# Kernel tuning notes

Hardware: AMD Instinct MI355X
Metric: run time of the kernel (lower is better)

Reference implementation:

```python
import jax, jax.numpy as jnp
from jax import lax
import numpy as np

NUM_TAGS = 128
BATCH = 256
SEQ = 1024


def setup_inputs() -> dict:
    key = jax.random.key(0)
    k1, k2, k3 = jax.random.split(key, 3)
    emissions = jax.random.normal(k1, (BATCH, SEQ, NUM_TAGS), dtype=jnp.float32)
    tags = jax.random.randint(k2, (BATCH, SEQ), 0, NUM_TAGS)
    mask = jnp.ones((BATCH, SEQ), dtype=jnp.float32)
    # xavier_uniform on [K,K] then clamp to [-1,1]
    limit = float(np.sqrt(6.0 / (NUM_TAGS + NUM_TAGS)))
    transitions = jnp.clip(
        jax.random.uniform(k3, (NUM_TAGS, NUM_TAGS), minval=-limit, maxval=limit),
        -1.0, 1.0).astype(jnp.float32)
    return {"emissions": emissions, "transitions": transitions, "tags": tags, "mask": mask}


def _log_partition(emissions, transitions, mask):
    # emissions: [B,S,K], mask: [B,S]
    alpha0 = emissions[:, 0]  # [B,K]
    emit_ts = jnp.swapaxes(emissions[:, 1:], 0, 1)  # [S-1,B,K]
    mask_ts = jnp.swapaxes(mask[:, 1:], 0, 1)       # [S-1,B]

    def step(alpha, xs):
        emit_t, mask_t = xs
        # [B,K,1] + [1,K,K] + [B,1,K] -> logsumexp over prev-tag axis
        new = jax.nn.logsumexp(alpha[:, :, None] + transitions[None, :, :] + emit_t[:, None, :], axis=1)
        alpha = jnp.where(mask_t[:, None].astype(bool), new, alpha)
        return alpha, None

    alpha, _ = lax.scan(step, alpha0, (emit_ts, mask_ts))
    return jax.nn.logsumexp(alpha, axis=1)  # [B]


def reference(emissions, transitions, tags, mask):
    # gold-path score
    emit_score = jnp.take_along_axis(emissions, tags[:, :, None], axis=2)[:, :, 0]  # [B,S]
    score = (emit_score * mask).sum(axis=1)
    trans_scores = transitions[tags[:, :-1], tags[:, 1:]] * mask[:, 1:]
    score = score + trans_scores.sum(axis=1)
    logZ = _log_partition(emissions, transitions, mask)
    return (logZ - score).mean()
```

## Files before the change

### kernel.cpp

```cpp
#include <hip/hip_runtime.h>
#include <stdint.h>

#define SEQ      1024
#define NT       128
#define NBATCH   256
#define MID      512
#define WS_STRIDE 132

typedef float v2f __attribute__((ext_vector_type(2)));

__global__ __launch_bounds__(256) void crf_chains(
    const float* __restrict__ emissions,
    const float* __restrict__ transitions,
    const int*   __restrict__ tags,
    const float* __restrict__ mask,
    float* __restrict__ out,
    float* __restrict__ ws)
{
    const int blk = blockIdx.x;
    const int tid = threadIdx.x;

    if (blk >= 2 * NBATCH) {
        int b    = (blk - 2 * NBATCH) * 4 + (tid >> 6);
        int lane = tid & 63;
        const float* emb = emissions + (size_t)b * SEQ * NT;
        const int*   tgb = tags + (size_t)b * SEQ;
        const float* mkb = mask + (size_t)b * SEQ;
        float sc = 0.f;
        for (int t = lane; t < SEQ; t += 64) {
            int   tg = tgb[t];
            float mt = mkb[t];
            sc += emb[t * NT + tg] * mt;
            if (t >= 1) sc += transitions[tgb[t - 1] * NT + tg] * mt;
        }
#pragma unroll
        for (int o = 32; o > 0; o >>= 1) sc += __shfl_down(sc, o, 64);
        if (lane == 0) atomicAdd(out, -sc * (1.0f / NBATCH));
        return;
    }

    const int jt = tid >> 1;
    const int q  = tid & 1;

    __shared__ __align__(16) float buf[2][NT];

#define MATVEC(Wt, S_) do { \
        v2f s0={0,0}, s1={0,0}, s2={0,0}, s3={0,0}; \
        _Pragma("unroll") \
        for (int cc = 0; cc < 8; ++cc) { \
            float4 ga = *(const float4*)(gp + cc * 8); \
            float4 gb = *(const float4*)(gp + cc * 8 + 4); \
            v2f a0 = {ga.x, ga.y}, a1 = {ga.z, ga.w}; \
            v2f b0 = {gb.x, gb.y}, b1 = {gb.z, gb.w}; \
            s0 = __builtin_elementwise_fma(Wt[4*cc+0], a0, s0); \
            s1 = __builtin_elementwise_fma(Wt[4*cc+1], a1, s1); \
            s2 = __builtin_elementwise_fma(Wt[4*cc+2], b0, s2); \
            s3 = __builtin_elementwise_fma(Wt[4*cc+3], b1, s3); \
        } \
        S_ = ((s0.x+s0.y)+(s1.x+s1.y)) + ((s2.x+s2.y)+(s3.x+s3.y)); \
        S_ += __shfl_xor(S_, 1, 64); \
    } while (0)

    if (blk < NBATCH) {
        const int b = blk;
        const float* emb = emissions + (size_t)b * SEQ * NT;
        const float* mkb = mask + (size_t)b * SEQ;

        v2f colT[32];
#pragma unroll
        for (int k = 0; k < 32; ++k) {
            int i = q * 64 + 2 * k;
            colT[k].x = __expf(transitions[(i    ) * NT + jt]);
            colT[k].y = __expf(transitions[(i + 1) * NT + jt]);
        }
        if (q == 0) buf[0][jt] = __expf(emb[jt]);
        __syncthreads();

        int kSum = 0, p = 0;
        float Ecur = emb[(1 + q) * NT + jt];
        float M0 = mkb[1], M1 = mkb[2];

        for (int t0 = 1; t0 < MID; t0 += 2) {
            float En  = emb[(t0 + 2 + q) * NT + jt];
            float Mn0 = mkb[t0 + 2];
            float Mn1 = mkb[t0 + 3];
#pragma unroll
            for (int dq = 0; dq < 2; ++dq) {
                float mt = dq ? M1 : M0;
                if (mt != 0.0f) {
                    float c0 = buf[p][0];
                    const float* gp = &buf[p][q * 64];
                    float s;
                    MATVEC(colT, s);
                    int k = (int)(__float_as_uint(c0) >> 23) - 127;
                    float rc = __uint_as_float((uint32_t)(127 - k) << 23);
                    kSum += k;
                    if (q == dq) buf[p ^ 1][jt] = s * rc * __expf(Ecur);
                    p ^= 1;
                }
                __syncthreads();
            }
            Ecur = En; M0 = Mn0; M1 = Mn1;
        }
        float* wsb = ws + (size_t)b * WS_STRIDE;
        if (q == 0)   wsb[jt]  = buf[p][jt];
        if (tid == 0) wsb[128] = (float)kSum;
        return;
    }

    {
        const int b = blk - NBATCH;
        const float* emb = emissions + (size_t)b * SEQ * NT;
        const float* mkb = mask + (size_t)b * SEQ;

        v2f rowT[32];
#pragma unroll
        for (int k = 0; k < 32; ++k) {
            int jj = q * 64 + 2 * k;
            rowT[k].x = __expf(transitions[jt * NT + jj]);
            rowT[k].y = __expf(transitions[jt * NT + jj + 1]);
        }
        if (q == 0) buf[0][jt] = __expf(emb[(size_t)(SEQ - 1) * NT + jt]);
        __syncthreads();

        int   kSum = 0, p = 0;
        float beta = 1.0f;
        float Ecur = emb[(size_t)(SEQ - 2 - q) * NT + jt];
        float M0 = mkb[SEQ - 1], M1 = mkb[SEQ - 2];

        for (int t0 = SEQ - 1; t0 >= MID + 1; t0 -= 2) {
            int tnE = t0 - 3 - q; if (tnE < 0) tnE = 0;
            float En  = emb[(size_t)tnE * NT + jt];
            int tm0 = t0 - 2; if (tm0 < 0) tm0 = 0;
            int tm1 = t0 - 3; if (tm1 < 0) tm1 = 0;
            float Mn0 = mkb[tm0], Mn1 = mkb[tm1];
#pragma unroll
            for (int dq = 0; dq < 2; ++dq) {
                int t = t0 - dq;
                if (t >= MID + 1) {
                    float mt = dq ? M1 : M0;
                    float c0 = buf[p][0];
                    const float* gp = &buf[p][q * 64];
                    float s;
                    MATVEC(rowT, s);
                    int k = (int)(__float_as_uint(c0) >> 23) - 127;
                    float rc = __uint_as_float((uint32_t)(127 - k) << 23);
                    kSum += k;
                    float bn = (mt != 0.0f) ? s * rc : beta * rc;
                    if (q == dq) buf[p ^ 1][jt] = bn * __expf(Ecur);
                    beta = bn; p ^= 1;
                    __syncthreads();
                }
            }
            Ecur = En; M0 = Mn0; M1 = Mn1;
        }
        float* wsb = ws + (size_t)(NBATCH + b) * WS_STRIDE;
        if (q == 0)   wsb[jt]  = beta;
        if (tid == 0) wsb[128] = (float)kSum;
        return;
    }
}

__global__ __launch_bounds__(64) void crf_combine(
    const float* __restrict__ ws, float* __restrict__ out)
{
    int b    = blockIdx.x;
    int lane = threadIdx.x;
    const float* af = ws + (size_t)b * WS_STRIDE;
    const float* bf = ws + (size_t)(NBATCH + b) * WS_STRIDE;
    float d = af[lane] * bf[lane] + af[lane + 64] * bf[lane + 64];
#pragma unroll
    for (int o = 32; o > 0; o >>= 1) d += __shfl_down(d, o, 64);
    if (lane == 0) {
        float logZ = __logf(d) + (af[128] + bf[128]) * 0.69314718055994531f;
        atomicAdd(out, logZ * (1.0f / NBATCH));
    }
}

extern "C" void kernel_launch(void* const* d_in, const int* in_sizes, int n_in,
                              void* d_out, int out_size, void* d_ws, size_t ws_size,
                              hipStream_t stream) {
    const float* emissions   = (const float*)d_in[0];
    const float* transitions = (const float*)d_in[1];
    const int*   tags        = (const int*)d_in[2];
    const float* mask        = (const float*)d_in[3];
    float*       out         = (float*)d_out;
    float*       ws          = (float*)d_ws;

    hipMemsetAsync(out, 0, sizeof(float), stream);
    crf_chains<<<2 * NBATCH + 64, 256, 0, stream>>>(
        emissions, transitions, tags, mask, out, ws);
    crf_combine<<<NBATCH, 64, 0, stream>>>(ws, out);
}
```

Baseline: 298.3 us.

## Fuse forward and backward chains into one block with full-row matvec per thread

```diff
diff --git a/kernel.cpp b/kernel.cpp
--- a/kernel.cpp
+++ b/kernel.cpp
@@ -8,6 +8,22 @@
 #define WS_STRIDE 132
 
 typedef float v2f __attribute__((ext_vector_type(2)));
+
+#define MATVEC128(S_) do { \
+        v2f s0={0,0}, s1={0,0}, s2={0,0}, s3={0,0}; \
+        _Pragma("unroll") \
+        for (int cc = 0; cc < 16; ++cc) { \
+            float4 ga = *(const float4*)(gp + cc * 8); \
+            float4 gb = *(const float4*)(gp + cc * 8 + 4); \
+            v2f a0 = {ga.x, ga.y}, a1 = {ga.z, ga.w}; \
+            v2f b0 = {gb.x, gb.y}, b1 = {gb.z, gb.w}; \
+            s0 = __builtin_elementwise_fma(Wv[4*cc+0], a0, s0); \
+            s1 = __builtin_elementwise_fma(Wv[4*cc+1], a1, s1); \
+            s2 = __builtin_elementwise_fma(Wv[4*cc+2], b0, s2); \
+            s3 = __builtin_elementwise_fma(Wv[4*cc+3], b1, s3); \
+        } \
+        S_ = ((s0.x+s0.y)+(s1.x+s1.y)) + ((s2.x+s2.y)+(s3.x+s3.y)); \
+    } while (0)
 
 __global__ __launch_bounds__(256) void crf_chains(
     const float* __restrict__ emissions,
@@ -20,8 +36,8 @@
     const int blk = blockIdx.x;
     const int tid = threadIdx.x;
 
-    if (blk >= 2 * NBATCH) {
-        int b    = (blk - 2 * NBATCH) * 4 + (tid >> 6);
+    if (blk >= NBATCH) {
+        int b    = (blk - NBATCH) * 4 + (tid >> 6);
         int lane = tid & 63;
         const float* emb = emissions + (size_t)b * SEQ * NT;
         const int*   tgb = tags + (size_t)b * SEQ;
@@ -39,125 +55,92 @@
         return;
     }
 
-    const int jt = tid >> 1;
-    const int q  = tid & 1;
+    __shared__ __align__(16) float bufF[2][NT];
+    __shared__ __align__(16) float bufB[2][NT];
 
-    __shared__ __align__(16) float buf[2][NT];
+    const int b    = blk;
+    const int half = tid >> 7;
+    const int jt   = tid & 127;
 
-#define MATVEC(Wt, S_) do { \
-        v2f s0={0,0}, s1={0,0}, s2={0,0}, s3={0,0}; \
-        _Pragma("unroll") \
-        for (int cc = 0; cc < 8; ++cc) { \
-            float4 ga = *(const float4*)(gp + cc * 8); \
-            float4 gb = *(const float4*)(gp + cc * 8 + 4); \
-            v2f a0 = {ga.x, ga.y}, a1 = {ga.z, ga.w}; \
-            v2f b0 = {gb.x, gb.y}, b1 = {gb.z, gb.w}; \
-            s0 = __builtin_elementwise_fma(Wt[4*cc+0], a0, s0); \
-            s1 = __builtin_elementwise_fma(Wt[4*cc+1], a1, s1); \
-            s2 = __builtin_elementwise_fma(Wt[4*cc+2], b0, s2); \
-            s3 = __builtin_elementwise_fma(Wt[4*cc+3], b1, s3); \
-        } \
-        S_ = ((s0.x+s0.y)+(s1.x+s1.y)) + ((s2.x+s2.y)+(s3.x+s3.y)); \
-        S_ += __shfl_xor(S_, 1, 64); \
-    } while (0)
+    const float* emb = emissions + (size_t)b * SEQ * NT;
+    const float* mkb = mask + (size_t)b * SEQ;
 
-    if (blk < NBATCH) {
-        const int b = blk;
-        const float* emb = emissions + (size_t)b * SEQ * NT;
-        const float* mkb = mask + (size_t)b * SEQ;
-
-        v2f colT[32];
+    v2f Wv[64];
+    if (half == 0) {
 #pragma unroll
-        for (int k = 0; k < 32; ++k) {
-            int i = q * 64 + 2 * k;
-            colT[k].x = __expf(transitions[(i    ) * NT + jt]);
-            colT[k].y = __expf(transitions[(i + 1) * NT + jt]);
+        for (int k = 0; k < 64; ++k) {
+            Wv[k].x = __expf(transitions[(2 * k    ) * NT + jt]);
+            Wv[k].y = __expf(transitions[(2 * k + 1) * NT + jt]);
         }
-        if (q == 0) buf[0][jt] = __expf(emb[jt]);
-        __syncthreads();
-
-        int kSum = 0, p = 0;
-        float Ecur = emb[(1 + q) * NT + jt];
-        float M0 = mkb[1], M1 = mkb[2];
-
-        for (int t0 = 1; t0 < MID; t0 += 2) {
-            float En  = emb[(t0 + 2 + q) * NT + jt];
-            float Mn0 = mkb[t0 + 2];
-            float Mn1 = mkb[t0 + 3];
+    } else {
 #pragma unroll
-            for (int dq = 0; dq < 2; ++dq) {
-                float mt = dq ? M1 : M0;
-                if (mt != 0.0f) {
-                    float c0 = buf[p][0];
-                    const float* gp = &buf[p][q * 64];
-                    float s;
-                    MATVEC(colT, s);
-                    int k = (int)(__float_as_uint(c0) >> 23) - 127;
-                    float rc = __uint_as_float((uint32_t)(127 - k) << 23);
-                    kSum += k;
-                    if (q == dq) buf[p ^ 1][jt] = s * rc * __expf(Ecur);
-                    p ^= 1;
-                }
-                __syncthreads();
-            }
-            Ecur = En; M0 = Mn0; M1 = Mn1;
+        for (int k = 0; k < 64; ++k) {
+            Wv[k].x = __expf(transitions[jt * NT + 2 * k]);
+            Wv[k].y = __expf(transitions[jt * NT + 2 * k + 1]);
         }
-        float* wsb = ws + (size_t)b * WS_STRIDE;
-        if (q == 0)   wsb[jt]  = buf[p][jt];
-        if (tid == 0) wsb[128] = (float)kSum;
-        return;
     }
 
-    {
-        const int b = blk - NBATCH;
-        const float* emb = emissions + (size_t)b * SEQ * NT;
-        const float* mkb = mask + (size_t)b * SEQ;
+    if (half == 0) bufF[0][jt] = __expf(emb[jt]);
+    else           bufB[0][jt] = __expf(emb[(size_t)(SEQ - 1) * NT + jt]);
+    __syncthreads();
 
-        v2f rowT[32];
-#pragma unroll
-        for (int k = 0; k < 32; ++k) {
-            int jj = q * 64 + 2 * k;
-            rowT[k].x = __expf(transitions[jt * NT + jj]);
-            rowT[k].y = __expf(transitions[jt * NT + jj + 1]);
+    int   kSum = 0, p = 0;
+    float beta = 1.0f;
+
+    float E0, E1, M0, M1;
+    if (half == 0) {
+        E0 = emb[1 * NT + jt];  E1 = emb[2 * NT + jt];
+        M0 = mkb[1];            M1 = mkb[2];
+    } else {
+        E0 = emb[(size_t)(SEQ - 2) * NT + jt];
+        E1 = emb[(size_t)(SEQ - 3) * NT + jt];
+        M0 = mkb[SEQ - 1];      M1 = mkb[SEQ - 2];
+    }
+
+    for (int it = 0; it < MID; ++it) {
+        float En, Mn;
+        if (half == 0) { En = emb[(size_t)(3 + it) * NT + jt];    Mn = mkb[3 + it]; }
+        else           { En = emb[(size_t)(1020 - it) * NT + jt]; Mn = mkb[1021 - it]; }
+
+        if (half == 0) {
+            float mt = M0;
+            if (mt != 0.0f) {
+                const float* gp = bufF[p];
+                float s;
+                MATVEC128(s);
+                float c0 = gp[0];
+                int   k  = (int)(__float_as_uint(c0) >> 23) - 127;
+                float rc = __uint_as_float((uint32_t)(127 - k) << 23);
+                kSum += k;
+                bufF[p ^ 1][jt] = s * rc * __expf(E0);
+                p ^= 1;
+            }
+            E0 = E1; E1 = En; M0 = M1; M1 = Mn;
+        } else if (it < MID - 1) {
+            float mt = M0;
+            const float* gp = bufB[p];
+            float s;
+            MATVEC128(s);
+            float c0 = gp[0];
+            int   k  = (int)(__float_as_uint(c0) >> 23) - 127;
+            float rc = __uint_as_float((uint32_t)(127 - k) << 23);
+            kSum += k;
+            float bn = (mt != 0.0f) ? s * rc : beta * rc;
+            beta = bn;
+            bufB[p ^ 1][jt] = bn * __expf(E0);
+            p ^= 1;
+            E0 = E1; E1 = En; M0 = M1; M1 = Mn;
         }
-        if (q == 0) buf[0][jt] = __expf(emb[(size_t)(SEQ - 1) * NT + jt]);
         __syncthreads();
+    }
 
-        int   kSum = 0, p = 0;
-        float beta = 1.0f;
-        float Ecur = emb[(size_t)(SEQ - 2 - q) * NT + jt];
-        float M0 = mkb[SEQ - 1], M1 = mkb[SEQ - 2];
-
-        for (int t0 = SEQ - 1; t0 >= MID + 1; t0 -= 2) {
-            int tnE = t0 - 3 - q; if (tnE < 0) tnE = 0;
-            float En  = emb[(size_t)tnE * NT + jt];
-            int tm0 = t0 - 2; if (tm0 < 0) tm0 = 0;
-            int tm1 = t0 - 3; if (tm1 < 0) tm1 = 0;
-            float Mn0 = mkb[tm0], Mn1 = mkb[tm1];
-#pragma unroll
-            for (int dq = 0; dq < 2; ++dq) {
-                int t = t0 - dq;
-                if (t >= MID + 1) {
-                    float mt = dq ? M1 : M0;
-                    float c0 = buf[p][0];
-                    const float* gp = &buf[p][q * 64];
-                    float s;
-                    MATVEC(rowT, s);
-                    int k = (int)(__float_as_uint(c0) >> 23) - 127;
-                    float rc = __uint_as_float((uint32_t)(127 - k) << 23);
-                    kSum += k;
-                    float bn = (mt != 0.0f) ? s * rc : beta * rc;
-                    if (q == dq) buf[p ^ 1][jt] = bn * __expf(Ecur);
-                    beta = bn; p ^= 1;
-                    __syncthreads();
-                }
-            }
-            Ecur = En; M0 = Mn0; M1 = Mn1;
-        }
-        float* wsb = ws + (size_t)(NBATCH + b) * WS_STRIDE;
-        if (q == 0)   wsb[jt]  = beta;
-        if (tid == 0) wsb[128] = (float)kSum;
-        return;
+    float* wsb = ws + (size_t)(half * NBATCH + b) * WS_STRIDE;
+    if (half == 0) {
+        wsb[jt] = bufF[p][jt];
+        if (jt == 0) wsb[128] = (float)kSum;
+    } else {
+        wsb[jt] = beta;
+        if (jt == 0) wsb[128] = (float)kSum;
     }
 }
 
@@ -188,7 +171,7 @@
     float*       ws          = (float*)d_ws;
 
     hipMemsetAsync(out, 0, sizeof(float), stream);
-    crf_chains<<<2 * NBATCH + 64, 256, 0, stream>>>(
+    crf_chains<<<NBATCH + 64, 256, 0, stream>>>(
         emissions, transitions, tags, mask, out, ws);
     crf_combine<<<NBATCH, 64, 0, stream>>>(ws, out);
 }
```

Measured after the change: 417.0 us. 39.8% more time.
